# Performance work log

Measured on AMD Instinct MI355X. Metric: run time of the kernel, lower is better.

The kernel has to match this reference:

```python
import jax, jax.numpy as jnp
import numpy as np

D_MODEL = 1024
NUM_HEADS = 16
DEPTH = D_MODEL // NUM_HEADS


def setup_inputs() -> dict:
    key = jax.random.key(0)
    ks = jax.random.split(key, 9)
    B, S = 2, 2048
    s = 1.0 / np.sqrt(D_MODEL)
    return {
        "x": jax.random.normal(ks[0], (B, S, D_MODEL), dtype=jnp.float32),
        "wq": jax.random.normal(ks[1], (D_MODEL, D_MODEL), dtype=jnp.float32) * s,
        "bq": jnp.zeros((D_MODEL,), dtype=jnp.float32),
        "wk": jax.random.normal(ks[2], (D_MODEL, D_MODEL), dtype=jnp.float32) * s,
        "bk": jnp.zeros((D_MODEL,), dtype=jnp.float32),
        "wv": jax.random.normal(ks[3], (D_MODEL, D_MODEL), dtype=jnp.float32) * s,
        "bv": jnp.zeros((D_MODEL,), dtype=jnp.float32),
        "wo": jax.random.normal(ks[4], (D_MODEL, D_MODEL), dtype=jnp.float32) * s,
        "bo": jnp.zeros((D_MODEL,), dtype=jnp.float32),
    }


def _split_heads(t):
    # [B, S, D] -> [B, H, S, depth]
    B, S, _ = t.shape
    return t.reshape(B, S, NUM_HEADS, DEPTH).transpose(0, 2, 1, 3)


def reference(x, wq, bq, wk, bk, wv, bv, wo, bo):
    B, S, _ = x.shape
    q = _split_heads(x @ wq + bq)
    k = _split_heads(x @ wk + bk)
    v = _split_heads(x @ wv + bv)
    scale = 1.0 / jnp.sqrt(jnp.asarray(DEPTH, dtype=x.dtype))
    logits = jnp.einsum("bhsd,bhtd->bhst", q, k) * scale  # [B,H,S,S]
    attn = jax.nn.softmax(logits, axis=-1)
    ctx = jnp.einsum("bhst,bhtd->bhsd", attn, v)  # [B,H,S,depth]
    concat = ctx.transpose(0, 2, 1, 3).reshape(B, S, D_MODEL)
    return concat @ wo + bo
```

## Files before the change

### kernel.cpp

```cpp
#include <hip/hip_runtime.h>
#include <hip/hip_bf16.h>

typedef __bf16 bf16;
typedef __bf16 bf16x4 __attribute__((ext_vector_type(4)));
typedef __bf16 bf16x8 __attribute__((ext_vector_type(8)));
typedef float f32x4 __attribute__((ext_vector_type(4)));

typedef __attribute__((address_space(3))) void lds_void;
typedef const __attribute__((address_space(1))) void gbl_void;

#define D_MODEL 1024
#define NHEAD 16
#define DEPTH 64
#define SEQ 2048
#define BATCH 2
#define NTOK (BATCH * SEQ)

#define Q_SCALE 0.18033688f

__global__ __launch_bounds__(256) void prep(const float* __restrict__ w0,
                                            const float* __restrict__ w1,
                                            const float* __restrict__ w2,
                                            const float* __restrict__ w3,
                                            const float* __restrict__ x,
                                            bf16* __restrict__ wtb,
                                            bf16* __restrict__ xb) {
    int z = blockIdx.z;
    int tx = threadIdx.x, ty = threadIdx.y;
    if (z < 4) {
        const float* w = (z == 0) ? w0 : (z == 1) ? w1 : (z == 2) ? w2 : w3;
        bf16* d = wtb + (size_t)z * D_MODEL * D_MODEL;
        __shared__ float tile[32][33];
        int c0 = blockIdx.x * 32;
        int r0 = blockIdx.y * 32;
#pragma unroll
        for (int i = 0; i < 4; i++)
            tile[ty + i * 8][tx] = w[(size_t)(r0 + ty + i * 8) * D_MODEL + c0 + tx];
        __syncthreads();
#pragma unroll
        for (int i = 0; i < 4; i++)
            d[(size_t)(c0 + ty + i * 8) * D_MODEL + r0 + tx] = (bf16)tile[tx][ty + i * 8];
    } else {
        int t = ty * 32 + tx;
        size_t i = ((size_t)(z - 4) * 1024 + blockIdx.y * 32 + blockIdx.x) * 256 + t;
        float4 v = ((const float4*)x)[i];
        bf16x4 o = {(bf16)v.x, (bf16)v.y, (bf16)v.z, (bf16)v.w};
        *(bf16x4*)&xb[i * 4] = o;
    }
}

__global__ __launch_bounds__(512, 2) void qkv_gemm(const bf16* __restrict__ xb,
                                                   const bf16* __restrict__ wtb,
                                                   const float* __restrict__ bq,
                                                   const float* __restrict__ bk,
                                                   const float* __restrict__ bv,
                                                   bf16* __restrict__ q,
                                                   bf16* __restrict__ k,
                                                   bf16* __restrict__ v) {
    __shared__ bf16 sm[65536];

    const int flat = blockIdx.x;
    const int wg = (flat & 7) * 24 + (flat >> 3);
    const int mt = wg & 15, nt = wg >> 4;
    const int row0 = mt << 8;
    const int z = nt >> 2;
    const int nb = (nt & 3) << 8;

    const int tid = threadIdx.x;
    const int lane = tid & 63, wave = tid >> 6;
    const int wm = wave >> 2, wn = wave & 3;
    const int quad = lane >> 4, l16 = lane & 15;
    const int kch = ((quad ^ ((l16 >> 1) & 3)) << 3);

    const int srow = lane >> 2;
    const int scg = (lane & 3) ^ ((lane >> 3) & 3);
    const int stDst = wave * 1024 + lane * 8;

    const bf16* Ag = xb + (size_t)(row0 + wave * 32 + srow) * D_MODEL + scg * 8;
    const bf16* Bg = wtb + (size_t)z * D_MODEL * D_MODEL
                   + (size_t)(nb + wave * 32 + srow) * D_MODEL + scg * 8;

    f32x4 acc[8][4] = {};
    bf16x8 bfr[4];

#define GLL(SRC, DST) __builtin_amdgcn_global_load_lds((gbl_void*)(SRC), (lds_void*)(DST), 16, 0, 0)
#define STG_A(T_, KQ_, BUF_) { \
    const bf16* s_ = Ag + (T_) * 64 + (KQ_) * 32; \
    bf16* d_ = sm + (BUF_) * 16384 + (KQ_) * 8192 + stDst; \
    GLL(s_, d_); GLL(s_ + 16 * D_MODEL, d_ + 512); }
#define STG_B(T_, KQ_, BUF_) { \
    const bf16* s_ = Bg + (T_) * 64 + (KQ_) * 32; \
    bf16* d_ = sm + 32768 + (BUF_) * 16384 + (KQ_) * 8192 + stDst; \
    GLL(s_, d_); GLL(s_ + 16 * D_MODEL, d_ + 512); }
#define WAIT6 { asm volatile("s_waitcnt vmcnt(6)" ::: "memory"); }
#define NOW

#define PHASE(BUF_, KQ_, MQ_, STG_STMT, WAIT_STMT) { \
    bf16x8 af[4]; \
    const int ab_ = (BUF_) * 16384 + (KQ_) * 8192 + (wm * 128 + (MQ_) * 64 + l16) * 32 + kch; \
    _Pragma("unroll") \
    for (int i_ = 0; i_ < 4; i_++) af[i_] = *(const bf16x8*)&sm[ab_ + i_ * 512]; \
    if ((MQ_) == 0) { \
        const int bb_ = 32768 + (BUF_) * 16384 + (KQ_) * 8192 + (wn * 64 + l16) * 32 + kch; \
        _Pragma("unroll") \
        for (int j_ = 0; j_ < 4; j_++) bfr[j_] = *(const bf16x8*)&sm[bb_ + j_ * 512]; \
    } \
    STG_STMT; \
    WAIT_STMT; \
    __builtin_amdgcn_sched_barrier(0); \
    __builtin_amdgcn_s_barrier(); \
    __builtin_amdgcn_s_setprio(1); \
    _Pragma("unroll") \
    for (int i_ = 0; i_ < 4; i_++) \
        _Pragma("unroll") \
        for (int j_ = 0; j_ < 4; j_++) \
            acc[(MQ_) * 4 + i_][j_] = __builtin_amdgcn_mfma_f32_16x16x32_bf16( \
                af[i_], bfr[j_], acc[(MQ_) * 4 + i_][j_], 0, 0, 0); \
    __builtin_amdgcn_s_setprio(0); \
    __builtin_amdgcn_sched_barrier(0); \
    __builtin_amdgcn_s_barrier(); }

    STG_B(0, 0, 0);
    STG_A(0, 0, 0);
    STG_B(0, 1, 0);
    STG_A(0, 1, 0);
    asm volatile("s_waitcnt vmcnt(4)" ::: "memory");
    STG_B(1, 0, 1);
    STG_A(1, 0, 1);
    STG_B(1, 1, 1);
    asm volatile("s_waitcnt vmcnt(6)" ::: "memory");
    __builtin_amdgcn_sched_barrier(0);
    __builtin_amdgcn_s_barrier();

#pragma unroll 1
    for (int it = 0; it < 8; ++it) {
        const int t1 = 2 * it + 1;
        const int t2 = (2 * it + 2) & 15;
        const int t3 = (2 * it + 3) & 15;
        PHASE(0, 0, 0, STG_A(t1, 1, 1), NOW)
        PHASE(0, 0, 1, STG_B(t2, 0, 0), NOW)
        PHASE(0, 1, 0, STG_A(t2, 0, 0), NOW)
        PHASE(0, 1, 1, STG_B(t2, 1, 0), WAIT6)
        PHASE(1, 0, 0, STG_A(t2, 1, 0), NOW)
        PHASE(1, 0, 1, STG_B(t3, 0, 1), NOW)
        PHASE(1, 1, 0, STG_A(t3, 0, 1), NOW)
        PHASE(1, 1, 1, STG_B(t3, 1, 1), WAIT6)
    }

#undef PHASE
#undef WAIT6
#undef NOW
#undef STG_A
#undef STG_B
#undef GLL

    const float* bias = (z == 0) ? bq : (z == 1) ? bk : bv;
    const int bI = row0 >> 11;
    const int sBase = row0 & 2047;
    if (z < 2) {
        bf16* dst = (z == 0) ? q : k;
        const float scl = (z == 0) ? Q_SCALE : 1.0f;
#pragma unroll
        for (int j = 0; j < 4; j++) {
            const int f = nb + wn * 64 + j * 16 + l16;
            const float bi = bias[f];
            const int hh = f >> 6, d = f & 63;
            bf16* dcol = dst + ((size_t)(bI * NHEAD + hh) * SEQ) * DEPTH + d;
#pragma unroll
            for (int mi = 0; mi < 8; mi++) {
                const int s0 = sBase + wm * 128 + (mi >> 2) * 64 + (mi & 3) * 16 + quad * 4;
#pragma unroll
                for (int r = 0; r < 4; r++)
                    dcol[(size_t)(s0 + r) * DEPTH] = (bf16)((acc[mi][j][r] + bi) * scl);
            }
        }
    } else {
#pragma unroll
        for (int j = 0; j < 4; j++) {
            const int f = nb + wn * 64 + j * 16 + l16;
            const float bi = bias[f];
            const int hh = f >> 6, d = f & 63;
            bf16* vrow = v + ((size_t)(bI * NHEAD + hh) * DEPTH + d) * SEQ;
#pragma unroll
            for (int mi = 0; mi < 8; mi++) {
                const int s0 = sBase + wm * 128 + (mi >> 2) * 64 + (mi & 3) * 16 + quad * 4;
                f32x4 a = acc[mi][j];
                bf16x4 ob = {(bf16)(a[0] + bi), (bf16)(a[1] + bi),
                             (bf16)(a[2] + bi), (bf16)(a[3] + bi)};
                *(bf16x4*)&vrow[s0] = ob;
            }
        }
    }
}

__global__ __launch_bounds__(512, 4) void attn(const bf16* __restrict__ q,
                                               const bf16* __restrict__ k,
                                               const bf16* __restrict__ v,
                                               bf16* __restrict__ ctx) {
    __shared__ __align__(16) bf16 smb[32768];
    const int tid = threadIdx.x;
    const int lane = tid & 63, wave = tid >> 6;
    const int ks = wave & 3, qg = wave >> 2;
    const int quad = lane >> 4, l16 = lane & 15;
    const int bh = blockIdx.x;
    const int q0 = blockIdx.y * 64;
    const size_t hb = (size_t)bh * SEQ * DEPTH;
    const bf16* qh = q + hb;
    const bf16* kh = k + hb;
    const bf16* vh = v + hb;

    bf16x8 bq_[2][2];
#pragma unroll
    for (int n = 0; n < 2; n++) {
        int qrow = q0 + qg * 32 + n * 16 + l16;
#pragma unroll
        for (int c = 0; c < 2; c++)
            bq_[n][c] = *(const bf16x8*)&qh[(size_t)qrow * DEPTH + c * 32 + quad * 8];
    }

    f32x4 ov[4][2] = {};
    float lvs[2] = {0.f, 0.f};

    const int sb = ks * 8192;
    const int kchS = (lane & 7) ^ (((lane >> 3) & 3) << 1);
    const int vchS = (lane & 3) ^ ((lane >> 3) & 3);
    const int krdL = ((l16 >> 2) << 3) + (l16 & 3);
    const int ksw = ((l16 & 3) << 1) | ((l16 >> 2) & 1);
    const int vsw = (quad ^ ((l16 >> 1) & 3)) << 3;

#define GLL(SRC, DST) __builtin_amdgcn_global_load_lds((gbl_void*)(SRC), (lds_void*)(DST), 16, 0, 0)

#define STAGE(BUF_, T_) { \
    _Pragma("unroll") \
    for (int o_ = 0; o_ < 4; o_++) { \
        const bf16* s_ = kh + (size_t)((T_) + ks * 32 + o_ * 8 + (lane >> 3)) * DEPTH \
                       + ((kchS ^ (o_ & 1)) << 3); \
        GLL(s_, smb + sb + (BUF_) * 2048 + o_ * 512 + lane * 8); \
    } \
    _Pragma("unroll") \
    for (int o_ = 0; o_ < 4; o_++) { \
        const bf16* s_ = vh + (size_t)(o_ * 16 + (lane >> 2)) * SEQ + (T_) + ks * 32 \
                       + (vchS << 3); \
        GLL(s_, smb + sb + 4096 + (BUF_) * 2048 + o_ * 512 + lane * 8); \
    } }

#define COMPUTE(BUF_) { \
    f32x4 s[2][2] = {}; \
    __builtin_amdgcn_s_setprio(1); \
    _Pragma("unroll") \
    for (int c_ = 0; c_ < 2; c_++) \
        _Pragma("unroll") \
        for (int h_ = 0; h_ < 2; h_++) { \
            bf16x8 kf = *(const bf16x8*)&smb[sb + (BUF_) * 2048 + (krdL + h_ * 4) * 64 \
                                             + ((((c_ << 2) | quad) ^ ksw) << 3)]; \
            _Pragma("unroll") \
            for (int n_ = 0; n_ < 2; n_++) \
                s[h_][n_] = __builtin_amdgcn_mfma_f32_16x16x32_bf16(kf, bq_[n_][c_], s[h_][n_], 0, 0, 0); \
        } \
    __builtin_amdgcn_s_setprio(0); \
    bf16x8 pb[2]; \
    _Pragma("unroll") \
    for (int n_ = 0; n_ < 2; n_++) { \
        float e0 = __builtin_amdgcn_exp2f(s[0][n_][0]); \
        float e1 = __builtin_amdgcn_exp2f(s[0][n_][1]); \
        float e2 = __builtin_amdgcn_exp2f(s[0][n_][2]); \
        float e3 = __builtin_amdgcn_exp2f(s[0][n_][3]); \
        float e4 = __builtin_amdgcn_exp2f(s[1][n_][0]); \
        float e5 = __builtin_amdgcn_exp2f(s[1][n_][1]); \
        float e6 = __builtin_amdgcn_exp2f(s[1][n_][2]); \
        float e7 = __builtin_amdgcn_exp2f(s[1][n_][3]); \
        pb[n_][0] = (bf16)e0; pb[n_][1] = (bf16)e1; \
        pb[n_][2] = (bf16)e2; pb[n_][3] = (bf16)e3; \
        pb[n_][4] = (bf16)e4; pb[n_][5] = (bf16)e5; \
        pb[n_][6] = (bf16)e6; pb[n_][7] = (bf16)e7; \
        lvs[n_] += ((e0 + e1) + (e2 + e3)) + ((e4 + e5) + (e6 + e7)); \
    } \
    __builtin_amdgcn_s_setprio(1); \
    _Pragma("unroll") \
    for (int t_ = 0; t_ < 4; t_++) { \
        bf16x8 vf = *(const bf16x8*)&smb[sb + 4096 + (BUF_) * 2048 + (t_ * 16 + l16) * 32 + vsw]; \
        _Pragma("unroll") \
        for (int n_ = 0; n_ < 2; n_++) \
            ov[t_][n_] = __builtin_amdgcn_mfma_f32_16x16x32_bf16(vf, pb[n_], ov[t_][n_], 0, 0, 0); \
    } \
    __builtin_amdgcn_s_setprio(0); }

#define SB0 __builtin_amdgcn_sched_barrier(0)

    if (qg == 0) STAGE(0, 0);
#pragma unroll 1
    for (int i = 0; i < 16; i++) {
        if (qg == 0) {
            if (i < 15) {
                STAGE((i + 1) & 1, (i + 1) * 128);
                asm volatile("s_waitcnt vmcnt(8)" ::: "memory");
            } else {
                asm volatile("s_waitcnt vmcnt(0)" ::: "memory");
            }
        }
        SB0;
        __builtin_amdgcn_s_barrier();
        COMPUTE(i & 1);
        SB0;
        __builtin_amdgcn_s_barrier();
    }

#undef SB0
#undef COMPUTE
#undef STAGE
#undef GLL

    f32x4* Red  = (f32x4*)smb;
    float* Lred = (float*)((char*)smb + 32768);
    const int b = bh >> 4, hh = bh & 15;
    const int tA = ks >> 1, nA = ks & 1;

    __syncthreads();
#pragma unroll
    for (int t2 = 0; t2 < 2; t2++)
#pragma unroll
        for (int n = 0; n < 2; n++)
            Red[((((qg * 2 + t2) * 2 + n) * 4) + ks) * 64 + lane] = ov[t2][n];
#pragma unroll
    for (int n = 0; n < 2; n++)
        Lred[((qg * 2 + n) * 4 + ks) * 64 + lane] = lvs[n];
    __syncthreads();

    float ls0 = 0.f, ls1 = 0.f;
#pragma unroll
    for (int k4 = 0; k4 < 4; k4++)
#pragma unroll
        for (int qd = 0; qd < 4; qd++) {
            ls0 += Lred[((qg * 2 + 0) * 4 + k4) * 64 + qd * 16 + l16];
            ls1 += Lred[((qg * 2 + 1) * 4 + k4) * 64 + qd * 16 + l16];
        }
    const float lsn = (ks & 1) ? ls1 : ls0;
    const float iv = 1.0f / lsn;

    {
        f32x4 sv = Red[((((qg * 2 + tA) * 2 + nA) * 4) + 0) * 64 + lane]
                 + Red[((((qg * 2 + tA) * 2 + nA) * 4) + 1) * 64 + lane]
                 + Red[((((qg * 2 + tA) * 2 + nA) * 4) + 2) * 64 + lane]
                 + Red[((((qg * 2 + tA) * 2 + nA) * 4) + 3) * 64 + lane];
        bf16x4 ob = {(bf16)(sv[0] * iv), (bf16)(sv[1] * iv),
                     (bf16)(sv[2] * iv), (bf16)(sv[3] * iv)};
        size_t off = ((size_t)(b * SEQ + q0 + qg * 32 + nA * 16 + l16)) * D_MODEL
                   + hh * 64 + tA * 16 + quad * 4;
        *(bf16x4*)&ctx[off] = ob;
    }
    __syncthreads();
#pragma unroll
    for (int t2 = 0; t2 < 2; t2++)
#pragma unroll
        for (int n = 0; n < 2; n++)
            Red[((((qg * 2 + t2) * 2 + n) * 4) + ks) * 64 + lane] = ov[2 + t2][n];
    __syncthreads();
    {
        f32x4 sv = Red[((((qg * 2 + tA) * 2 + nA) * 4) + 0) * 64 + lane]
                 + Red[((((qg * 2 + tA) * 2 + nA) * 4) + 1) * 64 + lane]
                 + Red[((((qg * 2 + tA) * 2 + nA) * 4) + 2) * 64 + lane]
                 + Red[((((qg * 2 + tA) * 2 + nA) * 4) + 3) * 64 + lane];
        bf16x4 ob = {(bf16)(sv[0] * iv), (bf16)(sv[1] * iv),
                     (bf16)(sv[2] * iv), (bf16)(sv[3] * iv)};
        size_t off = ((size_t)(b * SEQ + q0 + qg * 32 + nA * 16 + l16)) * D_MODEL
                   + hh * 64 + (2 + tA) * 16 + quad * 4;
        *(bf16x4*)&ctx[off] = ob;
    }
}

__global__ __launch_bounds__(256) void out_gemm(const bf16* __restrict__ ctx,
                                                const bf16* __restrict__ wot,
                                                const float* __restrict__ bo,
                                                float* __restrict__ out) {
    __shared__ bf16 As[64 * 32];
    __shared__ bf16 Bs[128 * 32];
    const int tid = threadIdx.x;
    const int lane = tid & 63, wave = tid >> 6;
    const int quad = lane >> 4, l16 = lane & 15;
    const int srow = lane >> 2, selem = (lane & 3) * 8;
    int row0 = blockIdx.y * 64, col0 = blockIdx.x * 128;
    f32x4 acc[4][2] = {};

    for (int k0 = 0; k0 < D_MODEL; k0 += 32) {
        __syncthreads();
        {
            const bf16* ga = ctx + (size_t)(row0 + wave * 16 + srow) * D_MODEL + k0 + selem;
            __builtin_amdgcn_global_load_lds((gbl_void*)ga, (lds_void*)(As + wave * 512 + lane * 8), 16, 0, 0);
        }
#pragma unroll
        for (int t = 0; t < 2; t++) {
            int m = wave * 2 + t;
            const bf16* gb = wot + (size_t)(col0 + m * 16 + srow) * D_MODEL + k0 + selem;
            __builtin_amdgcn_global_load_lds((gbl_void*)gb, (lds_void*)(Bs + m * 512 + lane * 8), 16, 0, 0);
        }
        __syncthreads();
        bf16x8 af[4], bfr[2];
#pragma unroll
        for (int i = 0; i < 4; i++)
            af[i] = *(const bf16x8*)&As[(i * 16 + l16) * 32 + quad * 8];
#pragma unroll
        for (int j = 0; j < 2; j++)
            bfr[j] = *(const bf16x8*)&Bs[(wave * 32 + j * 16 + l16) * 32 + quad * 8];
#pragma unroll
        for (int i = 0; i < 4; i++)
#pragma unroll
            for (int j = 0; j < 2; j++)
                acc[i][j] = __builtin_amdgcn_mfma_f32_16x16x32_bf16(af[i], bfr[j], acc[i][j], 0, 0, 0);
    }
#pragma unroll
    for (int i = 0; i < 4; i++)
#pragma unroll
        for (int j = 0; j < 2; j++) {
            int colg = col0 + wave * 32 + j * 16 + l16;
            float bi = bo[colg];
            int rbase = row0 + i * 16 + quad * 4;
#pragma unroll
            for (int r = 0; r < 4; r++)
                out[(size_t)(rbase + r) * D_MODEL + colg] = acc[i][j][r] + bi;
        }
}

extern "C" void kernel_launch(void* const* d_in, const int* in_sizes, int n_in,
                              void* d_out, int out_size, void* d_ws, size_t ws_size,
                              hipStream_t stream) {
    const float* x  = (const float*)d_in[0];
    const float* wq = (const float*)d_in[1];
    const float* bq = (const float*)d_in[2];
    const float* wk = (const float*)d_in[3];
    const float* bk = (const float*)d_in[4];
    const float* wv = (const float*)d_in[5];
    const float* bv = (const float*)d_in[6];
    const float* wo = (const float*)d_in[7];
    const float* bo = (const float*)d_in[8];
    float* out = (float*)d_out;

    const size_t MB = 1024 * 1024;
    char* ws = (char*)d_ws;
    bf16* xb  = (bf16*)(ws);
    bf16* wtb = (bf16*)(ws + 8 * MB);
    bf16* qb  = (bf16*)(ws + 16 * MB);
    bf16* kb  = (bf16*)(ws + 24 * MB);
    bf16* vb  = (bf16*)(ws + 32 * MB);
    bf16* ctx = (bf16*)(ws + 40 * MB);

    prep<<<dim3(32, 32, 8), dim3(32, 8), 0, stream>>>(wq, wk, wv, wo, x, wtb, xb);
    qkv_gemm<<<dim3(192), dim3(512), 0, stream>>>(xb, wtb, bq, bk, bv, qb, kb, vb);
    attn<<<dim3(BATCH * NHEAD, SEQ / 64), dim3(512), 0, stream>>>(qb, kb, vb, ctx);
    out_gemm<<<dim3(8, 64), 256, 0, stream>>>(ctx, wtb + 3 * (size_t)D_MODEL * D_MODEL, bo, out);
}
```

Measured before the change: 189.5 us.

## Replace 256x256 QKV GEMM with shared 128x128 double-buffered core

The hand-scheduled 256x256-tile QKV GEMM with 512 threads and a phased, interleaved staging pipeline is replaced by a simpler templated 128x128 core that uses 256 threads and a plain two-stage double buffer over 64-wide K slices. The grid grows from 192 to 768 blocks, which helps spread work across the many compute units. For V the MFMA operands are swapped so the transposed store lands on contiguous tokens, but each element is still stored as a scalar. The cost is less data reuse per tile and a less finely overlapped load/compute schedule.

```diff
diff --git a/kernel.cpp b/kernel.cpp
--- a/kernel.cpp
+++ b/kernel.cpp
@@ -49,145 +49,126 @@
     }
 }
 
-__global__ __launch_bounds__(512, 2) void qkv_gemm(const bf16* __restrict__ xb,
-                                                   const bf16* __restrict__ wtb,
-                                                   const float* __restrict__ bq,
-                                                   const float* __restrict__ bk,
-                                                   const float* __restrict__ bv,
-                                                   bf16* __restrict__ q,
-                                                   bf16* __restrict__ k,
-                                                   bf16* __restrict__ v) {
-    __shared__ bf16 sm[65536];
-
-    const int flat = blockIdx.x;
-    const int wg = (flat & 7) * 24 + (flat >> 3);
-    const int mt = wg & 15, nt = wg >> 4;
-    const int row0 = mt << 8;
-    const int z = nt >> 2;
-    const int nb = (nt & 3) << 8;
-
+template <bool SWAP>
+__device__ __forceinline__ void gemm_core128(const bf16* __restrict__ A,
+                                             const bf16* __restrict__ Bt,
+                                             int row0, int col0,
+                                             bf16 (*sm)[2][8192],
+                                             f32x4 acc[4][4]) {
     const int tid = threadIdx.x;
-    const int lane = tid & 63, wave = tid >> 6;
-    const int wm = wave >> 2, wn = wave & 3;
+    const int lane = tid & 63;
+    const int wave = tid >> 6;
     const int quad = lane >> 4, l16 = lane & 15;
-    const int kch = ((quad ^ ((l16 >> 1) & 3)) << 3);
-
-    const int srow = lane >> 2;
-    const int scg = (lane & 3) ^ ((lane >> 3) & 3);
-    const int stDst = wave * 1024 + lane * 8;
-
-    const bf16* Ag = xb + (size_t)(row0 + wave * 32 + srow) * D_MODEL + scg * 8;
-    const bf16* Bg = wtb + (size_t)z * D_MODEL * D_MODEL
-                   + (size_t)(nb + wave * 32 + srow) * D_MODEL + scg * 8;
-
-    f32x4 acc[8][4] = {};
-    bf16x8 bfr[4];
-
-#define GLL(SRC, DST) __builtin_amdgcn_global_load_lds((gbl_void*)(SRC), (lds_void*)(DST), 16, 0, 0)
-#define STG_A(T_, KQ_, BUF_) { \
-    const bf16* s_ = Ag + (T_) * 64 + (KQ_) * 32; \
-    bf16* d_ = sm + (BUF_) * 16384 + (KQ_) * 8192 + stDst; \
-    GLL(s_, d_); GLL(s_ + 16 * D_MODEL, d_ + 512); }
-#define STG_B(T_, KQ_, BUF_) { \
-    const bf16* s_ = Bg + (T_) * 64 + (KQ_) * 32; \
-    bf16* d_ = sm + 32768 + (BUF_) * 16384 + (KQ_) * 8192 + stDst; \
-    GLL(s_, d_); GLL(s_ + 16 * D_MODEL, d_ + 512); }
-#define WAIT6 { asm volatile("s_waitcnt vmcnt(6)" ::: "memory"); }
-#define NOW
-
-#define PHASE(BUF_, KQ_, MQ_, STG_STMT, WAIT_STMT) { \
-    bf16x8 af[4]; \
-    const int ab_ = (BUF_) * 16384 + (KQ_) * 8192 + (wm * 128 + (MQ_) * 64 + l16) * 32 + kch; \
-    _Pragma("unroll") \
-    for (int i_ = 0; i_ < 4; i_++) af[i_] = *(const bf16x8*)&sm[ab_ + i_ * 512]; \
-    if ((MQ_) == 0) { \
-        const int bb_ = 32768 + (BUF_) * 16384 + (KQ_) * 8192 + (wn * 64 + l16) * 32 + kch; \
-        _Pragma("unroll") \
-        for (int j_ = 0; j_ < 4; j_++) bfr[j_] = *(const bf16x8*)&sm[bb_ + j_ * 512]; \
-    } \
-    STG_STMT; \
-    WAIT_STMT; \
-    __builtin_amdgcn_sched_barrier(0); \
-    __builtin_amdgcn_s_barrier(); \
-    __builtin_amdgcn_s_setprio(1); \
-    _Pragma("unroll") \
-    for (int i_ = 0; i_ < 4; i_++) \
-        _Pragma("unroll") \
-        for (int j_ = 0; j_ < 4; j_++) \
-            acc[(MQ_) * 4 + i_][j_] = __builtin_amdgcn_mfma_f32_16x16x32_bf16( \
-                af[i_], bfr[j_], acc[(MQ_) * 4 + i_][j_], 0, 0, 0); \
-    __builtin_amdgcn_s_setprio(0); \
-    __builtin_amdgcn_sched_barrier(0); \
-    __builtin_amdgcn_s_barrier(); }
-
-    STG_B(0, 0, 0);
-    STG_A(0, 0, 0);
-    STG_B(0, 1, 0);
-    STG_A(0, 1, 0);
-    asm volatile("s_waitcnt vmcnt(4)" ::: "memory");
-    STG_B(1, 0, 1);
-    STG_A(1, 0, 1);
-    STG_B(1, 1, 1);
-    asm volatile("s_waitcnt vmcnt(6)" ::: "memory");
-    __builtin_amdgcn_sched_barrier(0);
-    __builtin_amdgcn_s_barrier();
-
+    const int wm = (wave & 1) << 6, wn = (wave >> 1) << 6;
+    const int sA = l16 & 7;
+    const int scg = (tid & 7) ^ ((tid >> 3) & 7);
+
+    const bf16* Ag = A + (size_t)(row0 + (tid >> 3)) * D_MODEL + scg * 8;
+    const bf16* Bg = Bt + (size_t)(col0 + (tid >> 3)) * D_MODEL + scg * 8;
+
+#define GLLQ(SRC, DST) __builtin_amdgcn_global_load_lds((gbl_void*)(SRC), (lds_void*)(DST), 16, 0, 0)
+#define STGQ(BUF_, KB_) { \
+    _Pragma("unroll") \
+    for (int o_ = 0; o_ < 4; o_++) \
+        GLLQ(Ag + (size_t)o_ * 32 * D_MODEL + (KB_), &sm[BUF_][0][o_ * 2048 + tid * 8]); \
+    _Pragma("unroll") \
+    for (int o_ = 0; o_ < 4; o_++) \
+        GLLQ(Bg + (size_t)o_ * 32 * D_MODEL + (KB_), &sm[BUF_][1][o_ * 2048 + tid * 8]); }
+
+    STGQ(0, 0);
 #pragma unroll 1
-    for (int it = 0; it < 8; ++it) {
-        const int t1 = 2 * it + 1;
-        const int t2 = (2 * it + 2) & 15;
-        const int t3 = (2 * it + 3) & 15;
-        PHASE(0, 0, 0, STG_A(t1, 1, 1), NOW)
-        PHASE(0, 0, 1, STG_B(t2, 0, 0), NOW)
-        PHASE(0, 1, 0, STG_A(t2, 0, 0), NOW)
-        PHASE(0, 1, 1, STG_B(t2, 1, 0), WAIT6)
-        PHASE(1, 0, 0, STG_A(t2, 1, 0), NOW)
-        PHASE(1, 0, 1, STG_B(t3, 0, 1), NOW)
-        PHASE(1, 1, 0, STG_A(t3, 0, 1), NOW)
-        PHASE(1, 1, 1, STG_B(t3, 1, 1), WAIT6)
-    }
-
-#undef PHASE
-#undef WAIT6
-#undef NOW
-#undef STG_A
-#undef STG_B
-#undef GLL
-
+    for (int t = 0; t < 16; t++) {
+        if (t < 15) {
+            STGQ((t + 1) & 1, (t + 1) * 64);
+            asm volatile("s_waitcnt vmcnt(8)" ::: "memory");
+        } else {
+            asm volatile("s_waitcnt vmcnt(0)" ::: "memory");
+        }
+        __builtin_amdgcn_sched_barrier(0);
+        __builtin_amdgcn_s_barrier();
+        const int bs = t & 1;
+#pragma unroll
+        for (int kq = 0; kq < 2; kq++) {
+            bf16x8 af[4], bfr[4];
+            const int c = ((((kq << 2) | quad) ^ sA) << 3);
+#pragma unroll
+            for (int i = 0; i < 4; i++)
+                af[i] = *(const bf16x8*)&sm[bs][0][(wm + i * 16 + l16) * 64 + c];
+#pragma unroll
+            for (int j = 0; j < 4; j++)
+                bfr[j] = *(const bf16x8*)&sm[bs][1][(wn + j * 16 + l16) * 64 + c];
+            __builtin_amdgcn_s_setprio(1);
+#pragma unroll
+            for (int i = 0; i < 4; i++)
+#pragma unroll
+                for (int j = 0; j < 4; j++)
+                    acc[i][j] = SWAP
+                        ? __builtin_amdgcn_mfma_f32_16x16x32_bf16(bfr[j], af[i], acc[i][j], 0, 0, 0)
+                        : __builtin_amdgcn_mfma_f32_16x16x32_bf16(af[i], bfr[j], acc[i][j], 0, 0, 0);
+            __builtin_amdgcn_s_setprio(0);
+        }
+        __builtin_amdgcn_sched_barrier(0);
+        __builtin_amdgcn_s_barrier();
+    }
+#undef STGQ
+#undef GLLQ
+}
+
+__global__ __launch_bounds__(256) void qkv_gemm(const bf16* __restrict__ xb,
+                                                const bf16* __restrict__ wtb,
+                                                const float* __restrict__ bq,
+                                                const float* __restrict__ bk,
+                                                const float* __restrict__ bv,
+                                                bf16* __restrict__ q,
+                                                bf16* __restrict__ k,
+                                                bf16* __restrict__ v) {
+    __shared__ __align__(16) bf16 sm[2][2][8192];
+    int zc = blockIdx.x;
+    int z = zc >> 3;
+    const bf16* Bt = wtb + (size_t)z * D_MODEL * D_MODEL;
     const float* bias = (z == 0) ? bq : (z == 1) ? bk : bv;
-    const int bI = row0 >> 11;
-    const int sBase = row0 & 2047;
+    int row0 = blockIdx.y * 128, col0 = (zc & 7) * 128;
+    f32x4 acc[4][4] = {};
+
+    const int lane = threadIdx.x & 63, wave = threadIdx.x >> 6;
+    const int quad = lane >> 4, l16 = lane & 15;
+    const int wm = (wave & 1) << 6, wn = (wave >> 1) << 6;
+
     if (z < 2) {
+        gemm_core128<false>(xb, Bt, row0, col0, sm, acc);
         bf16* dst = (z == 0) ? q : k;
-        const float scl = (z == 0) ? Q_SCALE : 1.0f;
-#pragma unroll
-        for (int j = 0; j < 4; j++) {
-            const int f = nb + wn * 64 + j * 16 + l16;
-            const float bi = bias[f];
-            const int hh = f >> 6, d = f & 63;
-            bf16* dcol = dst + ((size_t)(bI * NHEAD + hh) * SEQ) * DEPTH + d;
-#pragma unroll
-            for (int mi = 0; mi < 8; mi++) {
-                const int s0 = sBase + wm * 128 + (mi >> 2) * 64 + (mi & 3) * 16 + quad * 4;
-#pragma unroll
-                for (int r = 0; r < 4; r++)
-                    dcol[(size_t)(s0 + r) * DEPTH] = (bf16)((acc[mi][j][r] + bi) * scl);
+        const float sc = (z == 0) ? Q_SCALE : 1.0f;
+#pragma unroll
+        for (int i = 0; i < 4; i++) {
+#pragma unroll
+            for (int j = 0; j < 4; j++) {
+                int colg = col0 + wn + j * 16 + l16;
+                int hh = colg >> 6, d = colg & 63;
+                float bi = bias[colg];
+                int rbase = row0 + wm + i * 16 + quad * 4;
+                int b = rbase >> 11, sb = rbase & 2047;
+#pragma unroll
+                for (int r = 0; r < 4; r++) {
+                    size_t idx = ((size_t)(b * NHEAD + hh) * SEQ + sb + r) * DEPTH + d;
+                    dst[idx] = (bf16)((acc[i][j][r] + bi) * sc);
+                }
             }
         }
     } else {
-#pragma unroll
-        for (int j = 0; j < 4; j++) {
-            const int f = nb + wn * 64 + j * 16 + l16;
-            const float bi = bias[f];
-            const int hh = f >> 6, d = f & 63;
-            bf16* vrow = v + ((size_t)(bI * NHEAD + hh) * DEPTH + d) * SEQ;
-#pragma unroll
-            for (int mi = 0; mi < 8; mi++) {
-                const int s0 = sBase + wm * 128 + (mi >> 2) * 64 + (mi & 3) * 16 + quad * 4;
-                f32x4 a = acc[mi][j];
-                bf16x4 ob = {(bf16)(a[0] + bi), (bf16)(a[1] + bi),
-                             (bf16)(a[2] + bi), (bf16)(a[3] + bi)};
-                *(bf16x4*)&vrow[s0] = ob;
+        gemm_core128<true>(xb, Bt, row0, col0, sm, acc);
+#pragma unroll
+        for (int i = 0; i < 4; i++) {
+            int tok = row0 + wm + i * 16 + l16;
+            int b = tok >> 11, sb = tok & 2047;
+#pragma unroll
+            for (int j = 0; j < 4; j++) {
+#pragma unroll
+                for (int r = 0; r < 4; r++) {
+                    int f = col0 + wn + j * 16 + quad * 4 + r;
+                    int hh = f >> 6, d = f & 63;
+                    v[((size_t)(b * NHEAD + hh) * DEPTH + d) * SEQ + sb] =
+                        (bf16)(acc[i][j][r] + bias[f]);
+                }
             }
         }
     }
@@ -444,7 +425,7 @@
     bf16* ctx = (bf16*)(ws + 40 * MB);
 
     prep<<<dim3(32, 32, 8), dim3(32, 8), 0, stream>>>(wq, wk, wv, wo, x, wtb, xb);
-    qkv_gemm<<<dim3(192), dim3(512), 0, stream>>>(xb, wtb, bq, bk, bv, qb, kb, vb);
+    qkv_gemm<<<dim3(24, 32), 256, 0, stream>>>(xb, wtb, bq, bk, bv, qb, kb, vb);
     attn<<<dim3(BATCH * NHEAD, SEQ / 64), dim3(512), 0, stream>>>(qb, kb, vb, ctx);
     out_gemm<<<dim3(8, 64), 256, 0, stream>>>(ctx, wtb + 3 * (size_t)D_MODEL * D_MODEL, bo, out);
 }
```

After: 184.6 us, median of 2. -2.6%, faster.
